# Optimization experiments

Hardware: AMD Instinct MI355X
Metric: run time of the kernel (lower is better)

## Reference

```python
import jax, jax.numpy as jnp
import numpy as np

B, D = 8192, 256
MARGIN_MIN, MARGIN_MAX = 0.2, 0.5
EPS = 1e-8


def setup_inputs() -> dict:
    key = jax.random.key(0)
    ks = jax.random.split(key, 6)
    return {
        "vision_embeds_cross": jax.random.normal(ks[0], (B, D), jnp.float32),
        "text_embeds_cross": jax.random.normal(ks[1], (B, D), jnp.float32),
        "vision_embeds_uni": jax.random.normal(ks[2], (B, D), jnp.float32),
        "text_embeds_uni": jax.random.normal(ks[3], (B, D), jnp.float32),
        # itm_head: Linear(2D+1 -> D), ReLU, Linear(D -> 1)  (dropout off / eval)
        "W1": jax.random.normal(ks[4], (2 * D + 1, D), jnp.float32) * 0.02,
        "b1": jnp.zeros((D,), jnp.float32),
        "W2": jax.random.normal(ks[5], (D, 1), jnp.float32) * 0.02,
        "b2": jnp.zeros((1,), jnp.float32),
    }


def _mine_negatives(text_uni, vision_uni):
    """Vectorized semi-hard negative mining: one random in-band candidate per row,
    falling back to the hardest (argmax) off-diagonal negative when the band is empty."""
    S = text_uni @ vision_uni.T                      # [B, B]
    diag = jnp.diagonal(S)                           # [B]
    eye = jnp.eye(S.shape[0], dtype=bool)
    band = (S > diag[:, None] - MARGIN_MAX) & (S < diag[:, None] - MARGIN_MIN) & (~eye)
    # uniform random sampling among masked candidates via random-key argmax
    noise = jax.random.uniform(jax.random.key(42), S.shape, jnp.float32)
    sampled = jnp.argmax(jnp.where(band, noise, -1.0), axis=1)
    fallback = jnp.argmax(jnp.where(eye, -jnp.inf, S), axis=1)
    has_cand = band.any(axis=1)
    return jnp.where(has_cand, sampled, fallback)    # [B] int


def _itm_head(t, v, W1, b1, W2, b2):
    dot = jnp.sum(t * v, axis=-1, keepdims=True)     # [B, 1]
    x = jnp.concatenate([t, v, dot], axis=-1)        # [B, 2D+1]
    h = jax.nn.relu(x @ W1 + b1)                     # [B, D]
    return (h @ W2 + b2).squeeze(-1)                 # [B]


def reference(vision_embeds_cross, text_embeds_cross, vision_embeds_uni,
              text_embeds_uni, W1, b1, W2, b2):
    neg_idx = _mine_negatives(text_embeds_uni, vision_embeds_uni)
    logits_pos = _itm_head(text_embeds_cross, vision_embeds_cross, W1, b1, W2, b2)
    vision_neg = vision_embeds_cross[neg_idx]
    logits_neg = _itm_head(text_embeds_cross, vision_neg, W1, b1, W2, b2)
    pos_loss = -jnp.log(jax.nn.sigmoid(logits_pos) + EPS).mean()
    neg_loss = -jnp.log(1.0 - jax.nn.sigmoid(logits_neg) + EPS).mean()
    return (pos_loss + neg_loss) / 2.0
```

## Files before the change

kernel.cpp:

```cpp
#include <hip/hip_runtime.h>
#include <stdint.h>

#define NB 8192
#define DD 256

typedef unsigned short ushort_t;
typedef __attribute__((ext_vector_type(8))) short bf16x8;
typedef __attribute__((ext_vector_type(4))) float f32x4;

#define OFF_DIAG   0
#define OFF_NEG    32768
#define OFF_MROWS  65536
#define OFF_ACC    69632
#define OFF_BP1    73728
#define OFF_BP2    204800
#define OFF_FB2    335872
#define OFF_DIAG2  860160
#define OFF_A2     864256
#define OFF_W1T    1388544
#define OFF_TB     1650688
#define OFF_VB     5844992
#define OFF_TCB    10039296
#define OFF_VCB    14233600
#define WS_BIG     18427904

__device__ __forceinline__ unsigned short f2bf(float x) {
    uint32_t u = __float_as_uint(x);
    return (unsigned short)((u + 0x7FFFu + ((u >> 16) & 1u)) >> 16);
}

__device__ __forceinline__ uint4 packbf8(float4 x, float4 y) {
    uint4 o;
    o.x = (uint32_t)f2bf(x.x) | ((uint32_t)f2bf(x.y) << 16);
    o.y = (uint32_t)f2bf(x.z) | ((uint32_t)f2bf(x.w) << 16);
    o.z = (uint32_t)f2bf(y.x) | ((uint32_t)f2bf(y.y) << 16);
    o.w = (uint32_t)f2bf(y.z) | ((uint32_t)f2bf(y.w) << 16);
    return o;
}

__device__ __forceinline__ unsigned fkey(float s) {
    unsigned u = __float_as_uint(s);
    return (u & 0x80000000u) ? ~u : (u | 0x80000000u);
}

__device__ __forceinline__ void cvt_block(const float* __restrict__ in,
                                          ushort_t* __restrict__ out,
                                          int bsub, int tid) {
    int i = bsub * 256 + tid;
    int row = i >> 5, cw = i & 31, kb = cw >> 3, c = cw & 7;
    int csrc = c ^ (row & 7);
    const float4* src = (const float4*)(in + (size_t)row * DD + kb * 64 + csrc * 8);
    ((uint4*)out)[i] = packbf8(src[0], src[1]);
}

__global__ __launch_bounds__(256) void prep_uni_kernel(const float* __restrict__ t,
                                                       const float* __restrict__ v,
                                                       const float* __restrict__ tcross,
                                                       const float* __restrict__ vcross,
                                                       const float* __restrict__ W1,
                                                       ushort_t* __restrict__ tb,
                                                       ushort_t* __restrict__ vb,
                                                       ushort_t* __restrict__ tcb,
                                                       ushort_t* __restrict__ vcb,
                                                       ushort_t* __restrict__ W1T,
                                                       float* __restrict__ diag,
                                                       uint32_t* __restrict__ zeroRegion) {
    const int b = blockIdx.x;
    const int tid = threadIdx.x;
    if (b < 1024) {
        if (b == 0 && tid < 3) zeroRegion[tid] = 0;
        int r = b * 8 + (tid >> 5);
        int cw = tid & 31, kb = cw >> 3, c = cw & 7;
        int csrc = c ^ (r & 7);
        const float4* ts = (const float4*)(t + (size_t)r * DD + kb * 64 + csrc * 8);
        const float4* vs = (const float4*)(v + (size_t)r * DD + kb * 64 + csrc * 8);
        float4 t0 = ts[0], t1 = ts[1];
        float4 v0 = vs[0], v1 = vs[1];
        ((uint4*)tb)[(size_t)r * 32 + cw] = packbf8(t0, t1);
        ((uint4*)vb)[(size_t)r * 32 + cw] = packbf8(v0, v1);
        float s = t0.x * v0.x + t0.y * v0.y + t0.z * v0.z + t0.w * v0.w
                + t1.x * v1.x + t1.y * v1.y + t1.z * v1.z + t1.w * v1.w;
        #pragma unroll
        for (int off = 1; off < 32; off <<= 1) s += __shfl_xor(s, off);
        if ((tid & 31) == 0) diag[r] = s;
    } else if (b < 1056) {
        __shared__ float Ls[64][68];
        int tt = b - 1024;
        int kb = tt >> 2, nb = tt & 3;
        int r = tid >> 2, q4 = tid & 3;
        #pragma unroll
        for (int j = 0; j < 4; j++) {
            float4 x = *(const float4*)(W1 + (size_t)(kb * 64 + r) * DD + nb * 64 + q4 * 16 + j * 4);
            *(float4*)&Ls[r][q4 * 16 + j * 4] = x;
        }
        __syncthreads();
        int rn = tid >> 2, cq = (tid & 3) * 2;
        #pragma unroll
        for (int cc = 0; cc < 2; cc++) {
            int c = cq + cc;
            int csrc = c ^ (rn & 7);
            float4 x, y;
            x.x = Ls[csrc * 8 + 0][rn]; x.y = Ls[csrc * 8 + 1][rn];
            x.z = Ls[csrc * 8 + 2][rn]; x.w = Ls[csrc * 8 + 3][rn];
            y.x = Ls[csrc * 8 + 4][rn]; y.y = Ls[csrc * 8 + 5][rn];
            y.z = Ls[csrc * 8 + 6][rn]; y.w = Ls[csrc * 8 + 7][rn];
            *(uint4*)&W1T[(size_t)(nb * 64 + rn) * 512 + kb * 64 + c * 8] = packbf8(x, y);
        }
    } else {
        int bb = b - 1056;
        cvt_block((bb < 1024) ? tcross : vcross, (bb < 1024) ? tcb : vcb, bb & 1023, tid);
    }
}

__device__ __forceinline__ void stage_b(const ushort_t* __restrict__ VB, ushort_t* Bs,
                                        int colBase, int kc, int tid) {
    #pragma unroll
    for (int i = 0; i < 4; ++i) {
        int idx = i * 256 + tid;
        int r = idx >> 3, c8 = idx & 7;
        __builtin_amdgcn_global_load_lds(
            (const __attribute__((address_space(1))) uint32_t*)(VB + (size_t)(colBase + r) * DD + kc + c8 * 8),
            (__attribute__((address_space(3))) uint32_t*)(Bs + idx * 8), 16, 0, 0);
    }
}

__global__ __launch_bounds__(256, 4) void mine_p1_kernel(const ushort_t* __restrict__ TB,
                                                         const ushort_t* __restrict__ VB,
                                                         const float* __restrict__ diag,
                                                         ushort_t* __restrict__ bp1) {
    __shared__ ushort_t Bs[2][128 * 64];
    __shared__ float diag_s[128];

    const int tid = threadIdx.x;
    const int rowBase = blockIdx.x * 128;
    const int colBase = blockIdx.y * 128;
    const int lane = tid & 63;
    const int wave = tid >> 6;
    const int wr = wave >> 1, wc = wave & 1;
    const int lo = lane & 15, hi = lane >> 4;
    const int lx = lo & 7;

    if (tid < 128) diag_s[tid] = diag[rowBase + tid];

    f32x4 acc[4][4];
    #pragma unroll
    for (int m = 0; m < 4; m++)
        #pragma unroll
        for (int n = 0; n < 4; n++) acc[m][n] = (f32x4){0.f, 0.f, 0.f, 0.f};

    const ushort_t* Abase = TB + (size_t)(rowBase + wr * 64 + lo) * DD;

    stage_b(VB, Bs[0], colBase, 0, tid);
    __syncthreads();

    for (int kt = 0; kt < 4; ++kt) {
        const int buf = kt & 1;
        if (kt < 3)
            stage_b(VB, Bs[buf ^ 1], colBase, (kt + 1) * 64, tid);
        #pragma unroll
        for (int ksl = 0; ksl < 2; ksl++) {
            const int ch = ((((ksl << 2) | hi) ^ lx) << 3);
            bf16x8 a[4], b[4];
            #pragma unroll
            for (int m = 0; m < 4; m++)
                a[m] = *(const bf16x8*)(Abase + (size_t)m * 16 * DD + kt * 64 + ch);
            #pragma unroll
            for (int n = 0; n < 4; n++)
                b[n] = *(const bf16x8*)&Bs[buf][(wc * 64 + n * 16 + lo) * 64 + ch];
            #pragma unroll
            for (int m = 0; m < 4; m++)
                #pragma unroll
                for (int n = 0; n < 4; n++)
                    acc[m][n] = __builtin_amdgcn_mfma_f32_16x16x32_bf16(a[m], b[n], acc[m][n], 0, 0, 0);
        }
        __syncthreads();
    }

    #pragma unroll
    for (int m = 0; m < 4; m++) {
        #pragma unroll
        for (int q = 0; q < 4; q++) {
            const int rl = wr * 64 + m * 16 + hi * 4 + q;
            const int grow = rowBase + rl;
            const float c0 = diag_s[rl] - 0.35f;
            int bm = 0x7FFFFFFF;
            #pragma unroll
            for (int n = 0; n < 4; n++) {
                const float tt = acc[m][n][q] - c0;
                const int gcol = colBase + wc * 64 + n * 16 + lo;
                int cand = (fabsf(tt) < 0.15f && gcol != grow) ? gcol : 0x7FFFFFFF;
                bm = min(bm, cand);
            }
            #pragma unroll
            for (int off = 1; off < 16; off <<= 1) bm = min(bm, __shfl_xor(bm, off));
            if (lo == 0)
                bp1[blockIdx.y * NB + grow] = (ushort_t)min(bm, 0xFFFF);
        }
    }
}

__global__ __launch_bounds__(256) void combine_p1_kernel(const ushort_t* __restrict__ bp1,
                                                         const float* __restrict__ diag,
                                                         const ushort_t* __restrict__ TB,
                                                         int* __restrict__ neg,
                                                         int* __restrict__ mrows,
                                                         int* __restrict__ mcount,
                                                         ushort_t* __restrict__ A2,
                                                         float* __restrict__ diag2) {
    int row = blockIdx.x * 256 + threadIdx.x;
    int bmin = 0xFFFF;
    #pragma unroll
    for (int g = 0; g < 8; g++) bmin = min(bmin, (int)bp1[g * NB + row]);
    if (bmin < 0xFFFF) {
        neg[row] = bmin;
    } else {
        int i = atomicAdd(mcount, 1);
        if (i < 1024) {
            mrows[i] = row;
            neg[row] = -(i + 1);
            diag2[i] = diag[row];
            const uint4* src = (const uint4*)(TB + (size_t)row * DD);
            uint4* dst = (uint4*)(A2 + (size_t)i * DD);
            int kx = (i ^ row) & 7;
            #pragma unroll
            for (int cw = 0; cw < 32; cw++) {
                int kb = cw >> 3, c = cw & 7;
                dst[kb * 8 + c] = src[kb * 8 + (c ^ kx)];
            }
        } else {
            neg[row] = (row + 4096) & (NB - 1);
        }
    }
}

__global__ __launch_bounds__(256, 3) void mine_p2_kernel(const ushort_t* __restrict__ A2,
                                                         const ushort_t* __restrict__ VB,
                                                         const float* __restrict__ diag2,
                                                         const int* __restrict__ mrows,
                                                         const int* __restrict__ mcount,
                                                         ushort_t* __restrict__ bp2,
                                                         unsigned long long* __restrict__ fb2) {
    const int slotBase = blockIdx.x * 128;
    const int count = min(mcount[0], 1024);
    if (slotBase >= count) return;

    __shared__ ushort_t Bs[2][128 * 64];
    __shared__ float diag_s[128];
    __shared__ int rows_s[128];

    const int tid = threadIdx.x;
    const int colBase = blockIdx.y * 128;
    const int lane = tid & 63;
    const int wave = tid >> 6;
    const int wr = wave >> 1, wc = wave & 1;
    const int lo = lane & 15, hi = lane >> 4;
    const int lx = lo & 7;

    if (tid < 128) {
        diag_s[tid] = diag2[slotBase + tid];
        rows_s[tid] = mrows[slotBase + tid];
    }

    f32x4 acc[4][4];
    #pragma unroll
    for (int m = 0; m < 4; m++)
        #pragma unroll
        for (int n = 0; n < 4; n++) acc[m][n] = (f32x4){0.f, 0.f, 0.f, 0.f};

    const ushort_t* Abase = A2 + (size_t)(slotBase + wr * 64 + lo) * DD;

    stage_b(VB, Bs[0], colBase, 0, tid);
    __syncthreads();

    for (int kt = 0; kt < 4; ++kt) {
        const int buf = kt & 1;
        if (kt < 3)
            stage_b(VB, Bs[buf ^ 1], colBase, (kt + 1) * 64, tid);
        #pragma unroll
        for (int ksl = 0; ksl < 2; ksl++) {
            const int ch = ((((ksl << 2) | hi) ^ lx) << 3);
            bf16x8 a[4], b[4];
            #pragma unroll
            for (int m = 0; m < 4; m++)
                a[m] = *(const bf16x8*)(Abase + (size_t)m * 16 * DD + kt * 64 + ch);
            #pragma unroll
            for (int n = 0; n < 4; n++)
                b[n] = *(const bf16x8*)&Bs[buf][(wc * 64 + n * 16 + lo) * 64 + ch];
            #pragma unroll
            for (int m = 0; m < 4; m++)
                #pragma unroll
                for (int n = 0; n < 4; n++)
                    acc[m][n] = __builtin_amdgcn_mfma_f32_16x16x32_bf16(a[m], b[n], acc[m][n], 0, 0, 0);
        }
        __syncthreads();
    }

    #pragma unroll
    for (int m = 0; m < 4; m++) {
        #pragma unroll
        for (int q = 0; q < 4; q++) {
            const int rl = wr * 64 + m * 16 + hi * 4 + q;
            const int actual = rows_s[rl];
            const float c0 = diag_s[rl] - 0.35f;
            int bm = 0x7FFFFFFF;
            unsigned long long pk = 0ULL;
            #pragma unroll
            for (int n = 0; n < 4; n++) {
                const float s = acc[m][n][q];
                const int gcol = colBase + wc * 64 + n * 16 + lo;
                if (gcol != actual) {
                    unsigned long long p = ((unsigned long long)fkey(s) << 32) | (unsigned)(NB - 1 - gcol);
                    pk = (p > pk) ? p : pk;
                    if (fabsf(s - c0) < 0.15f) bm = min(bm, gcol);
                }
            }
            #pragma unroll
            for (int off = 1; off < 16; off <<= 1) {
                unsigned long long po = __shfl_xor(pk, off);
                int bo = __shfl_xor(bm, off);
                pk = (po > pk) ? po : pk;
                bm = min(bm, bo);
            }
            if (lo == 0) {
                bp2[blockIdx.y * 1024 + slotBase + rl] = (ushort_t)min(bm, 0xFFFF);
                fb2[blockIdx.y * 1024 + slotBase + rl] = pk;
            }
        }
    }
}

__global__ __launch_bounds__(256) void prep_head_kernel(const float* __restrict__ tcross,
                                                        const float* __restrict__ vcross,
                                                        ushort_t* __restrict__ tb,
                                                        ushort_t* __restrict__ vb) {
    const int b = blockIdx.x;
    cvt_block((b < 1024) ? tcross : vcross, (b < 1024) ? tb : vb, b & 1023, threadIdx.x);
}

__device__ __forceinline__ void stage_h4(const ushort_t* __restrict__ TCB,
                                         const ushort_t* __restrict__ VCB,
                                         const int* neg_l,
                                         const ushort_t* __restrict__ W1T,
                                         ushort_t* As, ushort_t* Bs,
                                         int rowBase, int kc, int tid) {
    if (kc < 256) {
        int r = tid >> 3, c8 = tid & 7;
        __builtin_amdgcn_global_load_lds(
            (const __attribute__((address_space(1))) uint32_t*)(TCB + (size_t)(rowBase + r) * DD + kc + c8 * 8),
            (__attribute__((address_space(3))) uint32_t*)(As + tid * 8), 16, 0, 0);
    } else {
        #pragma unroll
        for (int i = 0; i < 2; ++i) {
            int idx = i * 256 + tid;
            int r = idx >> 3, c8 = idx & 7;
            int rr = (r < 32) ? (rowBase + r) : neg_l[r - 32];
            int cs = c8 ^ ((r ^ rr) & 7);
            __builtin_amdgcn_global_load_lds(
                (const __attribute__((address_space(1))) uint32_t*)(VCB + (size_t)rr * DD + (kc - 256) + cs * 8),
                (__attribute__((address_space(3))) uint32_t*)(As + idx * 8), 16, 0, 0);
        }
    }
    #pragma unroll
    for (int i = 0; i < 8; ++i) {
        int idx = i * 256 + tid;
        int n = idx >> 3, c8 = idx & 7;
        __builtin_amdgcn_global_load_lds(
            (const __attribute__((address_space(1))) uint32_t*)(W1T + (size_t)n * 512 + kc + c8 * 8),
            (__attribute__((address_space(3))) uint32_t*)(Bs + idx * 8), 16, 0, 0);
    }
}

__global__ __launch_bounds__(256) void head4_kernel(const ushort_t* __restrict__ TCB,
                                                    const ushort_t* __restrict__ VCB,
                                                    const ushort_t* __restrict__ W1T,
                                                    const int* __restrict__ neg,
                                                    const ushort_t* __restrict__ bp2,
                                                    const unsigned long long* __restrict__ fb2,
                                                    const float* __restrict__ tcf,
                                                    const float* __restrict__ vcf,
                                                    const float* __restrict__ W1,
                                                    const float* __restrict__ b1,
                                                    const float* __restrict__ W2,
                                                    const float* __restrict__ b2,
                                                    float* __restrict__ acc_out,
                                                    int* __restrict__ hcount,
                                                    float* __restrict__ out) {
    __shared__ ushort_t As[2][64 * 64];
    __shared__ ushort_t Bs[2][256 * 64];
    __shared__ int neg_l[32];
    __shared__ float dotp_l[32], dotn_l[32];
    __shared__ float logit_p[32], logit_n[32];

    const int tid = threadIdx.x;
    const int rowBase = blockIdx.x * 32;
    const int lane = tid & 63;
    const int wcv = tid >> 6;
    const int lo = lane & 15, hi = lane >> 4;
    const int lx = lo & 7;

    if (tid < 32) {
        int grow = rowBase + tid;
        int nv = neg[grow];
        if (nv < 0) {
            int s = -nv - 1;
            int bmin = 0xFFFF;
            unsigned long long pk = 0ULL;
            #pragma unroll
            for (int g = 0; g < 64; g++) {
                bmin = min(bmin, (int)bp2[g * 1024 + s]);
                unsigned long long f = fb2[g * 1024 + s];
                pk = (f > pk) ? f : pk;
            }
            nv = (bmin < 0xFFFF) ? bmin : (NB - 1 - (int)(unsigned)(pk & 0xFFFFFFFFull));
        }
        neg_l[tid] = nv;
        logit_p[tid] = 0.f;
        logit_n[tid] = 0.f;
    }
    __syncthreads();

    stage_h4(TCB, VCB, neg_l, W1T, As[0], Bs[0], rowBase, 0, tid);

    {
        int r = tid >> 3, e = tid & 7;
        int grow = rowBase + r;
        int vn = neg_l[r];
        const float4* tp = (const float4*)(tcf + (size_t)grow * DD + e * 32);
        const float4* vp = (const float4*)(vcf + (size_t)grow * DD + e * 32);
        const float4* vq = (const float4*)(vcf + (size_t)vn * DD + e * 32);
        float sp = 0.f, sn = 0.f;
        #pragma unroll
        for (int j = 0; j < 8; j++) {
            float4 a = tp[j], v = vp[j], w = vq[j];
            sp += a.x * v.x + a.y * v.y + a.z * v.z + a.w * v.w;
            sn += a.x * w.x + a.y * w.y + a.z * w.z + a.w * w.w;
        }
        #pragma unroll
        for (int off = 1; off < 8; off <<= 1) {
            sp += __shfl_xor(sp, off);
            sn += __shfl_xor(sn, off);
        }
        if (e == 0) { dotp_l[r] = sp; dotn_l[r] = sn; }
    }

    f32x4 acc_t[2][4], acc_p[2][4], acc_n[2][4];
    #pragma unroll
    for (int m = 0; m < 2; m++)
        #pragma unroll
        for (int n = 0; n < 4; n++) {
            acc_t[m][n] = (f32x4){0.f, 0.f, 0.f, 0.f};
            acc_p[m][n] = (f32x4){0.f, 0.f, 0.f, 0.f};
            acc_n[m][n] = (f32x4){0.f, 0.f, 0.f, 0.f};
        }

    __syncthreads();

    for (int kt = 0; kt < 8; ++kt) {
        const int buf = kt & 1;
        if (kt < 7)
            stage_h4(TCB, VCB, neg_l, W1T, As[buf ^ 1], Bs[buf ^ 1], rowBase, (kt + 1) * 64, tid);
        #pragma unroll
        for (int ksl = 0; ksl < 2; ksl++) {
            const int ch = ((((ksl << 2) | hi) ^ lx) << 3);
            bf16x8 b[4];
            #pragma unroll
            for (int n = 0; n < 4; n++)
                b[n] = *(const bf16x8*)&Bs[buf][(wcv * 64 + n * 16 + lo) * 64 + ch];
            if (kt < 4) {
                bf16x8 a[2];
                #pragma unroll
                for (int m = 0; m < 2; m++)
                    a[m] = *(const bf16x8*)&As[buf][(m * 16 + lo) * 64 + ch];
                #pragma unroll
                for (int m = 0; m < 2; m++)
                    #pragma unroll
                    for (int n = 0; n < 4; n++)
                        acc_t[m][n] = __builtin_amdgcn_mfma_f32_16x16x32_bf16(a[m], b[n], acc_t[m][n], 0, 0, 0);
            } else {
                bf16x8 ap[2], an[2];
                #pragma unroll
                for (int m = 0; m < 2; m++) {
                    ap[m] = *(const bf16x8*)&As[buf][(m * 16 + lo) * 64 + ch];
                    an[m] = *(const bf16x8*)&As[buf][(32 + m * 16 + lo) * 64 + ch];
                }
                #pragma unroll
                for (int m = 0; m < 2; m++)
                    #pragma unroll
                    for (int n = 0; n < 4; n++) {
                        acc_p[m][n] = __builtin_amdgcn_mfma_f32_16x16x32_bf16(ap[m], b[n], acc_p[m][n], 0, 0, 0);
                        acc_n[m][n] = __builtin_amdgcn_mfma_f32_16x16x32_bf16(an[m], b[n], acc_n[m][n], 0, 0, 0);
                    }
            }
        }
        __syncthreads();
    }

    float b1v[4], w5v[4], w2v[4];
    #pragma unroll
    for (int n = 0; n < 4; n++) {
        int cl = wcv * 64 + n * 16 + lo;
        b1v[n] = b1[cl];
        w5v[n] = W1[(size_t)512 * DD + cl];
        w2v[n] = W2[cl];
    }
    #pragma unroll
    for (int m = 0; m < 2; m++) {
        #pragma unroll
        for (int q = 0; q < 4; q++) {
            const int rl = m * 16 + hi * 4 + q;
            const float dtp = dotp_l[rl], dtn = dotn_l[rl];
            float xp = 0.f, xn = 0.f;
            #pragma unroll
            for (int n = 0; n < 4; n++) {
                float base = acc_t[m][n][q] + b1v[n];
                float hp = base + acc_p[m][n][q] + dtp * w5v[n];
                float hn = base + acc_n[m][n][q] + dtn * w5v[n];
                xp += fmaxf(hp, 0.f) * w2v[n];
                xn += fmaxf(hn, 0.f) * w2v[n];
            }
            #pragma unroll
            for (int off = 1; off < 16; off <<= 1) {
                xp += __shfl_xor(xp, off);
                xn += __shfl_xor(xn, off);
            }
            if (lo == 0) {
                atomicAdd(&logit_p[rl], xp);
                atomicAdd(&logit_n[rl], xn);
            }
        }
    }
    __syncthreads();

    if (tid < 32) {
        float bb = b2[0];
        float xp = logit_p[tid] + bb;
        float xn = logit_n[tid] + bb;
        float term = -logf(1.f / (1.f + expf(-xp)) + 1e-8f)
                     -logf(1.f / (1.f + expf(xn)) + 1e-8f);
        #pragma unroll
        for (int off = 16; off; off >>= 1) term += __shfl_down(term, off);
        if (tid == 0) {
            atomicAdd(acc_out, term);
            __threadfence();
            int done = atomicAdd(hcount, 1);
            if (done == (int)gridDim.x - 1) {
                float total = atomicAdd(acc_out, 0.f);
                out[0] = total * (1.0f / (2.0f * (float)NB));
            }
        }
    }
}

extern "C" void kernel_launch(void* const* d_in, const int* in_sizes, int n_in,
                              void* d_out, int out_size, void* d_ws, size_t ws_size,
                              hipStream_t stream) {
    const float* vcross = (const float*)d_in[0];
    const float* tcross = (const float*)d_in[1];
    const float* vuni   = (const float*)d_in[2];
    const float* tuni   = (const float*)d_in[3];
    const float* W1     = (const float*)d_in[4];
    const float* b1     = (const float*)d_in[5];
    const float* W2     = (const float*)d_in[6];
    const float* b2     = (const float*)d_in[7];

    char* ws = (char*)d_ws;
    float* diag   = (float*)(ws + OFF_DIAG);
    int* neg      = (int*)(ws + OFF_NEG);
    int* mrows    = (int*)(ws + OFF_MROWS);
    float* acc    = (float*)(ws + OFF_ACC);
    int* mcount   = (int*)(ws + OFF_ACC + 4);
    int* hcount   = (int*)(ws + OFF_ACC + 8);
    ushort_t* bp1 = (ushort_t*)(ws + OFF_BP1);
    ushort_t* bp2 = (ushort_t*)(ws + OFF_BP2);
    unsigned long long* fb2 = (unsigned long long*)(ws + OFF_FB2);
    float* diag2  = (float*)(ws + OFF_DIAG2);
    ushort_t* A2  = (ushort_t*)(ws + OFF_A2);
    ushort_t* w1t = (ushort_t*)(ws + OFF_W1T);
    ushort_t* tb  = (ushort_t*)(ws + OFF_TB);
    ushort_t* vb  = (ushort_t*)(ws + OFF_VB);

    const int big = (ws_size >= (size_t)WS_BIG);
    ushort_t* tcb = big ? (ushort_t*)(ws + OFF_TCB) : tb;
    ushort_t* vcb = big ? (ushort_t*)(ws + OFF_VCB) : vb;

    prep_uni_kernel<<<big ? 3104 : 1056, 256, 0, stream>>>(
        tuni, vuni, tcross, vcross, W1, tb, vb, tcb, vcb, w1t, diag,
        (uint32_t*)(ws + OFF_ACC));
    mine_p1_kernel<<<dim3(64, 8), 256, 0, stream>>>(tb, vb, diag, bp1);
    combine_p1_kernel<<<NB / 256, 256, 0, stream>>>(bp1, diag, tb, neg, mrows, mcount, A2, diag2);
    mine_p2_kernel<<<dim3(8, 64), 256, 0, stream>>>(A2, vb, diag2, mrows, mcount, bp2, fb2);
    if (!big)
        prep_head_kernel<<<2048, 256, 0, stream>>>(tcross, vcross, tb, vb);
    head4_kernel<<<NB / 32, 256, 0, stream>>>(tcb, vcb, w1t, neg, bp2, fb2,
                                              tcross, vcross, W1, b1, W2, b2,
                                              acc, hcount, (float*)d_out);
}
```

Baseline: 72.75 us.

## Fuse cross-embedding bf16 conversion into head kernel A-tile staging

Removes the separate fp32-to-bf16 conversion of the cross embeddings (done in prep or a dedicated prep_head kernel). The head kernel now loads fp32 rows straight from the cross inputs into registers, converts them to bf16 and writes the swizzled A tiles into LDS after the MFMA phase. This drops a full write and re-read of 8 MB of bf16 intermediates and shrinks the prep grid. In exchange, the head kernel reads twice as many bytes for A, holds more registers, and stages A through registers instead of async global-to-LDS loads.

After: 68.89 us. 1.06x faster.

```diff
diff --git a/kernel.cpp b/kernel.cpp
--- a/kernel.cpp
+++ b/kernel.cpp
@@ -20,9 +20,6 @@
 #define OFF_W1T    1388544
 #define OFF_TB     1650688
 #define OFF_VB     5844992
-#define OFF_TCB    10039296
-#define OFF_VCB    14233600
-#define WS_BIG     18427904
 
 __device__ __forceinline__ unsigned short f2bf(float x) {
     uint32_t u = __float_as_uint(x);
@@ -43,25 +40,11 @@
     return (u & 0x80000000u) ? ~u : (u | 0x80000000u);
 }
 
-__device__ __forceinline__ void cvt_block(const float* __restrict__ in,
-                                          ushort_t* __restrict__ out,
-                                          int bsub, int tid) {
-    int i = bsub * 256 + tid;
-    int row = i >> 5, cw = i & 31, kb = cw >> 3, c = cw & 7;
-    int csrc = c ^ (row & 7);
-    const float4* src = (const float4*)(in + (size_t)row * DD + kb * 64 + csrc * 8);
-    ((uint4*)out)[i] = packbf8(src[0], src[1]);
-}
-
 __global__ __launch_bounds__(256) void prep_uni_kernel(const float* __restrict__ t,
                                                        const float* __restrict__ v,
-                                                       const float* __restrict__ tcross,
-                                                       const float* __restrict__ vcross,
                                                        const float* __restrict__ W1,
                                                        ushort_t* __restrict__ tb,
                                                        ushort_t* __restrict__ vb,
-                                                       ushort_t* __restrict__ tcb,
-                                                       ushort_t* __restrict__ vcb,
                                                        ushort_t* __restrict__ W1T,
                                                        float* __restrict__ diag,
                                                        uint32_t* __restrict__ zeroRegion) {
@@ -83,7 +66,7 @@
         #pragma unroll
         for (int off = 1; off < 32; off <<= 1) s += __shfl_xor(s, off);
         if ((tid & 31) == 0) diag[r] = s;
-    } else if (b < 1056) {
+    } else {
         __shared__ float Ls[64][68];
         int tt = b - 1024;
         int kb = tt >> 2, nb = tt & 3;
@@ -106,9 +89,6 @@
             y.z = Ls[csrc * 8 + 6][rn]; y.w = Ls[csrc * 8 + 7][rn];
             *(uint4*)&W1T[(size_t)(nb * 64 + rn) * 512 + kb * 64 + c * 8] = packbf8(x, y);
         }
-    } else {
-        int bb = b - 1056;
-        cvt_block((bb < 1024) ? tcross : vcross, (bb < 1024) ? tcb : vcb, bb & 1023, tid);
     }
 }
 
@@ -329,37 +309,8 @@
     }
 }
 
-__global__ __launch_bounds__(256) void prep_head_kernel(const float* __restrict__ tcross,
-                                                        const float* __restrict__ vcross,
-                                                        ushort_t* __restrict__ tb,
-                                                        ushort_t* __restrict__ vb) {
-    const int b = blockIdx.x;
-    cvt_block((b < 1024) ? tcross : vcross, (b < 1024) ? tb : vb, b & 1023, threadIdx.x);
-}
-
-__device__ __forceinline__ void stage_h4(const ushort_t* __restrict__ TCB,
-                                         const ushort_t* __restrict__ VCB,
-                                         const int* neg_l,
-                                         const ushort_t* __restrict__ W1T,
-                                         ushort_t* As, ushort_t* Bs,
-                                         int rowBase, int kc, int tid) {
-    if (kc < 256) {
-        int r = tid >> 3, c8 = tid & 7;
-        __builtin_amdgcn_global_load_lds(
-            (const __attribute__((address_space(1))) uint32_t*)(TCB + (size_t)(rowBase + r) * DD + kc + c8 * 8),
-            (__attribute__((address_space(3))) uint32_t*)(As + tid * 8), 16, 0, 0);
-    } else {
-        #pragma unroll
-        for (int i = 0; i < 2; ++i) {
-            int idx = i * 256 + tid;
-            int r = idx >> 3, c8 = idx & 7;
-            int rr = (r < 32) ? (rowBase + r) : neg_l[r - 32];
-            int cs = c8 ^ ((r ^ rr) & 7);
-            __builtin_amdgcn_global_load_lds(
-                (const __attribute__((address_space(1))) uint32_t*)(VCB + (size_t)rr * DD + (kc - 256) + cs * 8),
-                (__attribute__((address_space(3))) uint32_t*)(As + idx * 8), 16, 0, 0);
-        }
-    }
+__device__ __forceinline__ void stage_B5(const ushort_t* __restrict__ W1T, ushort_t* Bs,
+                                         int kc, int tid) {
     #pragma unroll
     for (int i = 0; i < 8; ++i) {
         int idx = i * 256 + tid;
@@ -370,9 +321,7 @@
     }
 }
 
-__global__ __launch_bounds__(256) void head4_kernel(const ushort_t* __restrict__ TCB,
-                                                    const ushort_t* __restrict__ VCB,
-                                                    const ushort_t* __restrict__ W1T,
+__global__ __launch_bounds__(256) void head5_kernel(const ushort_t* __restrict__ W1T,
                                                     const int* __restrict__ neg,
                                                     const ushort_t* __restrict__ bp2,
                                                     const unsigned long long* __restrict__ fb2,
@@ -417,10 +366,17 @@
         logit_p[tid] = 0.f;
         logit_n[tid] = 0.f;
     }
+
+    stage_B5(W1T, Bs[0], 0, tid);
+    float4 p0, p1;
+    {
+        int r = tid >> 3, c8 = tid & 7;
+        int lc = c8 ^ (r & 7);
+        const float4* src = (const float4*)(tcf + (size_t)(rowBase + r) * DD + 0 + lc * 8);
+        p0 = src[0]; p1 = src[1];
+    }
+
     __syncthreads();
-
-    stage_h4(TCB, VCB, neg_l, W1T, As[0], Bs[0], rowBase, 0, tid);
-
     {
         int r = tid >> 3, e = tid & 7;
         int grow = rowBase + r;
@@ -443,6 +399,8 @@
         if (e == 0) { dotp_l[r] = sp; dotn_l[r] = sn; }
     }
 
+    *(uint4*)(As[0] + tid * 8) = packbf8(p0, p1);
+
     f32x4 acc_t[2][4], acc_p[2][4], acc_n[2][4];
     #pragma unroll
     for (int m = 0; m < 2; m++)
@@ -457,8 +415,28 @@
 
     for (int kt = 0; kt < 8; ++kt) {
         const int buf = kt & 1;
-        if (kt < 7)
-            stage_h4(TCB, VCB, neg_l, W1T, As[buf ^ 1], Bs[buf ^ 1], rowBase, (kt + 1) * 64, tid);
+        float4 a00, a01, a10, a11;
+        if (kt < 7) {
+            const int kc = (kt + 1) * 64;
+            if (kc < 256) {
+                int r = tid >> 3, c8 = tid & 7;
+                int lc = c8 ^ (r & 7);
+                const float4* src = (const float4*)(tcf + (size_t)(rowBase + r) * DD + kc + lc * 8);
+                a00 = src[0]; a01 = src[1];
+            } else {
+                int r0 = tid >> 3, c80 = tid & 7;
+                int lc0 = c80 ^ (r0 & 7);
+                const float4* s0 = (const float4*)(vcf + (size_t)(rowBase + r0) * DD + (kc - 256) + lc0 * 8);
+                a00 = s0[0]; a01 = s0[1];
+                int idx = 256 + tid;
+                int r1 = idx >> 3, c81 = idx & 7;
+                int rr = neg_l[r1 - 32];
+                int lc1 = c81 ^ (r1 & 7);
+                const float4* s1 = (const float4*)(vcf + (size_t)rr * DD + (kc - 256) + lc1 * 8);
+                a10 = s1[0]; a11 = s1[1];
+            }
+            stage_B5(W1T, Bs[buf ^ 1], kc, tid);
+        }
         #pragma unroll
         for (int ksl = 0; ksl < 2; ksl++) {
             const int ch = ((((ksl << 2) | hi) ^ lx) << 3);
@@ -492,6 +470,12 @@
                     }
             }
         }
+        if (kt < 7) {
+            const int kc = (kt + 1) * 64;
+            *(uint4*)(As[buf ^ 1] + tid * 8) = packbf8(a00, a01);
+            if (kc >= 256)
+                *(uint4*)(As[buf ^ 1] + (256 + tid) * 8) = packbf8(a10, a11);
+        }
         __syncthreads();
     }
 
@@ -579,19 +563,12 @@
     ushort_t* tb  = (ushort_t*)(ws + OFF_TB);
     ushort_t* vb  = (ushort_t*)(ws + OFF_VB);
 
-    const int big = (ws_size >= (size_t)WS_BIG);
-    ushort_t* tcb = big ? (ushort_t*)(ws + OFF_TCB) : tb;
-    ushort_t* vcb = big ? (ushort_t*)(ws + OFF_VCB) : vb;
-
-    prep_uni_kernel<<<big ? 3104 : 1056, 256, 0, stream>>>(
-        tuni, vuni, tcross, vcross, W1, tb, vb, tcb, vcb, w1t, diag,
-        (uint32_t*)(ws + OFF_ACC));
+    prep_uni_kernel<<<1056, 256, 0, stream>>>(tuni, vuni, W1, tb, vb, w1t, diag,
+                                              (uint32_t*)(ws + OFF_ACC));
     mine_p1_kernel<<<dim3(64, 8), 256, 0, stream>>>(tb, vb, diag, bp1);
     combine_p1_kernel<<<NB / 256, 256, 0, stream>>>(bp1, diag, tb, neg, mrows, mcount, A2, diag2);
     mine_p2_kernel<<<dim3(8, 64), 256, 0, stream>>>(A2, vb, diag2, mrows, mcount, bp2, fb2);
-    if (!big)
-        prep_head_kernel<<<2048, 256, 0, stream>>>(tcross, vcross, tb, vb);
-    head4_kernel<<<NB / 32, 256, 0, stream>>>(tcb, vcb, w1t, neg, bp2, fb2,
+    head5_kernel<<<NB / 32, 256, 0, stream>>>(w1t, neg, bp2, fb2,
                                               tcross, vcross, W1, b1, W2, b2,
                                               acc, hcount, (float*)d_out);
 }
```
